# Optimization experiments

Measured on AMD Instinct MI355X. Metric: run time of the kernel, lower is better.

## Reference

```python
import jax, jax.numpy as jnp
import numpy as np

BN_EPS = 1e-5
K = 16


def pairwise_sqdist(a, b):
    # a: (B,N,C), b: (B,M,C) -> (B,N,M)
    aa = jnp.sum(a * a, axis=-1)[:, :, None]
    bb = jnp.sum(b * b, axis=-1)[:, None, :]
    return aa + bb - 2.0 * jnp.einsum('bnc,bmc->bnm', a, b)


def knn_idx(pts, k):
    # pts: (B,N,C) -> (B,N,k) indices of k nearest points (incl. self)
    d = pairwise_sqdist(pts, pts)
    _, idx = jax.lax.top_k(-d, k)
    return idx


def gather_points(pts, idx):
    # pts: (B,N,C), idx: (B,N,k) -> (B,N,k,C)
    return jax.vmap(lambda p, i: p[i])(pts, idx)


def conv_bn(x, W, b, gm, bt, relu=True):
    # 1x1 Conv1d + BatchNorm1d (training-mode batch stats) [+ ReLU]
    # x: (B,Cin,N), W: (Cout,Cin)
    y = jnp.einsum('oc,bcn->bon', W, x) + b[None, :, None]
    mu = jnp.mean(y, axis=(0, 2), keepdims=True)
    var = jnp.var(y, axis=(0, 2), keepdims=True)
    y = (y - mu) / jnp.sqrt(var + BN_EPS) * gm[None, :, None] + bt[None, :, None]
    return jax.nn.relu(y) if relu else y


def graph_layer(x, W, b, gm, bt):
    # x: (B,C,N)
    ft = jnp.swapaxes(x, 1, 2)                # (B,N,C)
    idx = knn_idx(ft, K)                      # (B,N,k)
    knn_x = gather_points(ft, idx)            # (B,N,k,C)
    m = jnp.max(knn_x, axis=2)                # (B,N,C)
    return conv_bn(jnp.swapaxes(m, 1, 2), W, b, gm, bt, relu=True)


def setup_inputs() -> dict:
    key = jax.random.key(0)
    ks = jax.random.split(key, 8)
    B, N = 8, 2048
    d = {'x': jax.random.normal(ks[0], (B, N, 3), dtype=jnp.float32)}

    def conv_params(k, cout, cin):
        W = jax.random.normal(k, (cout, cin), dtype=jnp.float32) * 0.02
        return W, jnp.zeros((cout,), jnp.float32), jnp.ones((cout,), jnp.float32), jnp.zeros((cout,), jnp.float32)

    for name, k, co, ci in [('1', ks[1], 64, 12), ('2', ks[2], 64, 64), ('3', ks[3], 64, 64),
                            ('g1', ks[4], 128, 64), ('g2', ks[5], 1024, 128), ('4', ks[6], 512, 1024)]:
        W, b, gm, bt = conv_params(k, co, ci)
        d['W' + name] = W; d['b' + name] = b; d['gm' + name] = gm; d['bt' + name] = bt
    return d


def reference(x, W1, b1, gm1, bt1, W2, b2, gm2, bt2, W3, b3, gm3, bt3,
              Wg1, bg1, gmg1, btg1, Wg2, bg2, gmg2, btg2, W4, b4, gm4, bt4):
    # x: (B,N,3)
    idx = knn_idx(x, K)                       # (B,N,k)
    knn_x = gather_points(x, idx)             # (B,N,k,3)
    knn_x = knn_x - jnp.mean(knn_x, axis=2, keepdims=True)
    cov = jnp.einsum('bnkc,bnkd->bncd', knn_x, knn_x)      # (B,N,3,3)
    B, N = x.shape[0], x.shape[1]
    cov = cov.reshape(B, N, 9).transpose(0, 2, 1)          # (B,9,N)
    h = jnp.concatenate([jnp.swapaxes(x, 1, 2), cov], axis=1)  # (B,12,N)
    h = conv_bn(h, W1, b1, gm1, bt1)
    h = conv_bn(h, W2, b2, gm2, bt2)
    h = conv_bn(h, W3, b3, gm3, bt3)
    h = graph_layer(h, Wg1, bg1, gmg1, btg1)               # (B,128,N)
    h = graph_layer(h, Wg2, bg2, gmg2, btg2)               # (B,1024,N)
    h = conv_bn(h, W4, b4, gm4, bt4, relu=False)           # (B,512,N)
    return jnp.max(h, axis=-1)                             # (B,512)
```

## Files before the change

### kernel.cpp

```cpp
#include <hip/hip_runtime.h>
#include <math.h>

#define B_ 8
#define N_ 2048
#define KNN 16

typedef __attribute__((ext_vector_type(4))) float f32x4;
typedef __attribute__((ext_vector_type(8))) short bf16x8;
typedef __attribute__((ext_vector_type(8))) _Float16 f16x8;
typedef __attribute__((address_space(3))) unsigned int lds_u32_t;
typedef __attribute__((address_space(1))) const unsigned int glb_u32_t;

__device__ inline unsigned short f2bf(float f) {
    unsigned int x = __float_as_uint(f);
    unsigned int r = (x + 0x7fffu + ((x >> 16) & 1u)) >> 16;
    return (unsigned short)r;
}

__device__ inline unsigned int fflip(float f) {
    unsigned int u = __float_as_uint(f);
    return u ^ (0x80000000u | (unsigned int)((int)u >> 31));
}

__device__ inline unsigned long long shflx64(unsigned long long v, int m) {
    int lo = __shfl_xor((int)(unsigned int)(v & 0xffffffffull), m, 64);
    int hi = __shfl_xor((int)(unsigned int)(v >> 32), m, 64);
    return ((unsigned long long)(unsigned int)hi << 32) | (unsigned int)lo;
}

__device__ inline void ce(unsigned long long& a, unsigned long long& b) {
    bool c = a < b;
    unsigned long long lo = c ? a : b;
    unsigned long long hi = c ? b : a;
    a = lo;
    b = hi;
}

#define SORT16(q)                                                         \
    _Pragma("unroll") for (int kk_ = 2; kk_ <= 16; kk_ <<= 1)             \
    _Pragma("unroll") for (int jj_ = kk_ >> 1; jj_ > 0; jj_ >>= 1)        \
    _Pragma("unroll") for (int ii_ = 0; ii_ < 16; ii_++) {                \
        int ll_ = ii_ ^ jj_;                                              \
        if (ll_ > ii_) {                                                  \
            if ((ii_ & kk_) == 0) ce(q[ii_], q[ll_]);                     \
            else ce(q[ll_], q[ii_]);                                      \
        }                                                                 \
    }

#define MERGE16(q)                                                        \
    _Pragma("unroll") for (int jj_ = 8; jj_ > 0; jj_ >>= 1)               \
    _Pragma("unroll") for (int ii_ = 0; ii_ < 16; ii_++) {                \
        int ll_ = ii_ ^ jj_;                                              \
        if (ll_ > ii_) ce(q[ii_], q[ll_]);                                \
    }

#define TOP16OF32(kA, kB, q)                                              \
    SORT16(kA);                                                           \
    SORT16(kB);                                                           \
    _Pragma("unroll") for (int ii_ = 0; ii_ < 16; ii_++) {                \
        unsigned long long b_ = kB[15 - ii_];                             \
        q[ii_] = kA[ii_] < b_ ? kA[ii_] : b_;                             \
    }                                                                     \
    MERGE16(q);

#define EXTRACT16(q, op)                                                  \
    for (int r_ = 0; r_ < KNN; r_++) {                                    \
        unsigned long long mk_ = q[0];                                    \
        _Pragma("unroll") for (int s_ = 32; s_ > 0; s_ >>= 1) {           \
            unsigned long long ok_ = shflx64(mk_, s_);                    \
            if (ok_ < mk_) mk_ = ok_;                                     \
        }                                                                 \
        if (lane == 0) (op)[r_] = (int)(mk_ & 2047u);                     \
        bool pop_ = (q[0] == mk_);                                        \
        _Pragma("unroll") for (int t_ = 0; t_ < 15; t_++)                 \
            q[t_] = pop_ ? q[t_ + 1] : q[t_];                             \
        q[15] = pop_ ? ~0ull : q[15];                                     \
    }

__global__ __launch_bounds__(256, 4) void knn3_kernel(const float* __restrict__ x,
                                                      int* __restrict__ idx,
                                                      float* __restrict__ h0) {
    __shared__ float px[N_], py[N_], pz[N_];
    int b = blockIdx.y;
    const float* xb = x + (size_t)b * N_ * 3;
    for (int e = threadIdx.x; e < N_; e += 256) {
        px[e] = xb[e * 3 + 0];
        py[e] = xb[e * 3 + 1];
        pz[e] = xb[e * 3 + 2];
    }
    __syncthreads();

    int wave = threadIdx.x >> 6, lane = threadIdx.x & 63;
    int i = blockIdx.x * 4 + wave;
    float qx = px[i], qy = py[i], qz = pz[i];

    unsigned long long kA[16], kB[16];
#pragma unroll
    for (int t = 0; t < 16; t++) {
        int j = lane + t * 64;
        float dx = px[j] - qx, dy = py[j] - qy, dz = pz[j] - qz;
        float d = dx * dx + dy * dy + dz * dz;
        kA[t] = ((unsigned long long)fflip(d) << 11) | (unsigned int)j;
    }
#pragma unroll
    for (int t = 0; t < 16; t++) {
        int j = lane + (t + 16) * 64;
        float dx = px[j] - qx, dy = py[j] - qy, dz = pz[j] - qz;
        float d = dx * dx + dy * dy + dz * dz;
        kB[t] = ((unsigned long long)fflip(d) << 11) | (unsigned int)j;
    }

    unsigned long long q[16];
    TOP16OF32(kA, kB, q);

    int* op = idx + ((size_t)b * N_ + i) * KNN;
    unsigned int jr[16];
#pragma unroll
    for (int r_ = 0; r_ < KNN; r_++) {
        unsigned long long mk_ = q[0];
#pragma unroll
        for (int s_ = 32; s_ > 0; s_ >>= 1) {
            unsigned long long ok_ = shflx64(mk_, s_);
            if (ok_ < mk_) mk_ = ok_;
        }
        jr[r_] = (unsigned int)(mk_ & 2047u);
        if (lane == 0) op[r_] = (int)jr[r_];
        bool pop_ = (q[0] == mk_);
#pragma unroll
        for (int t_ = 0; t_ < 15; t_++) q[t_] = pop_ ? q[t_ + 1] : q[t_];
        q[15] = pop_ ? ~0ull : q[15];
    }

    float nx[16], ny[16], nz[16];
    float mx = 0.f, my = 0.f, mz = 0.f;
#pragma unroll
    for (int r_ = 0; r_ < 16; r_++) {
        int j = (int)jr[r_];
        nx[r_] = px[j]; ny[r_] = py[j]; nz[r_] = pz[j];
        mx += nx[r_]; my += ny[r_]; mz += nz[r_];
    }
    mx *= (1.f / KNN); my *= (1.f / KNN); mz *= (1.f / KNN);
    float c00 = 0, c01 = 0, c02 = 0, c11 = 0, c12 = 0, c22 = 0;
#pragma unroll
    for (int r_ = 0; r_ < 16; r_++) {
        float dx = nx[r_] - mx, dy = ny[r_] - my, dz = nz[r_] - mz;
        c00 += dx * dx; c01 += dx * dy; c02 += dx * dz;
        c11 += dy * dy; c12 += dy * dz; c22 += dz * dz;
    }
    if (lane == 0) {
        float* hb = h0 + (size_t)b * 12 * N_;
        hb[0 * N_ + i] = qx;
        hb[1 * N_ + i] = qy;
        hb[2 * N_ + i] = qz;
        hb[3 * N_ + i] = c00; hb[4 * N_ + i] = c01; hb[5 * N_ + i] = c02;
        hb[6 * N_ + i] = c01; hb[7 * N_ + i] = c11; hb[8 * N_ + i] = c12;
        hb[9 * N_ + i] = c02; hb[10 * N_ + i] = c12; hb[11 * N_ + i] = c22;
    }
}

__global__ __launch_bounds__(256) void gemm_kernel(const float* __restrict__ A,
                                                   const float* __restrict__ X,
                                                   const float* __restrict__ bias,
                                                   float* __restrict__ Y,
                                                   int O, int C,
                                                   float* __restrict__ part) {
    __shared__ float Wt[16][132];
    __shared__ float Xt[16][132];
    const int N = N_;
    int b = blockIdx.z;
    int oB = blockIdx.y * 128, nB = blockIdx.x * 128;
    const float* Xb = X + (size_t)b * C * N;
    int tid = threadIdx.x;
    int tn = tid & 15, to = tid >> 4;

    float acc[8][8];
#pragma unroll
    for (int i = 0; i < 8; i++)
#pragma unroll
        for (int j = 0; j < 8; j++) acc[i][j] = 0.f;

    for (int c0 = 0; c0 < C; c0 += 16) {
#pragma unroll
        for (int r = 0; r < 8; r++) {
            int e = tid + r * 256;
            int k = e & 15, o = e >> 4;
            float v = 0.f;
            if (c0 + k < C && oB + o < O) v = A[(size_t)(oB + o) * C + c0 + k];
            Wt[k][o] = v;
        }
#pragma unroll
        for (int r = 0; r < 8; r++) {
            int e = tid + r * 256;
            int n = e & 127, k = e >> 7;
            float v = 0.f;
            if (c0 + k < C) v = Xb[(size_t)(c0 + k) * N + nB + n];
            Xt[k][n] = v;
        }
        __syncthreads();
#pragma unroll
        for (int k = 0; k < 16; k++) {
            float a[8], xv[8];
#pragma unroll
            for (int i = 0; i < 8; i++) a[i] = Wt[k][to * 8 + i];
#pragma unroll
            for (int m = 0; m < 4; m++) {
                xv[2 * m] = Xt[k][tn * 2 + 32 * m];
                xv[2 * m + 1] = Xt[k][tn * 2 + 32 * m + 1];
            }
#pragma unroll
            for (int i = 0; i < 8; i++)
#pragma unroll
                for (int j = 0; j < 8; j++) acc[i][j] = fmaf(a[i], xv[j], acc[i][j]);
        }
        __syncthreads();
    }

#pragma unroll
    for (int i = 0; i < 8; i++) {
        int o = oB + to * 8 + i;
        if (o >= O) continue;
        float bv = bias[o];
        float s = 0.f, s2 = 0.f;
#pragma unroll
        for (int m = 0; m < 4; m++) {
            int n0 = nB + tn * 2 + 32 * m;
            float v0 = acc[i][2 * m] + bv, v1 = acc[i][2 * m + 1] + bv;
            *reinterpret_cast<float2*>(&Y[((size_t)b * O + o) * N + n0]) = make_float2(v0, v1);
            s += v0 + v1;
            s2 = fmaf(v0, v0, fmaf(v1, v1, s2));
        }
#pragma unroll
        for (int msk = 1; msk <= 8; msk <<= 1) {
            s += __shfl_xor(s, msk, 64);
            s2 += __shfl_xor(s2, msk, 64);
        }
        if (tn == 0) {
            float* pp = &part[((size_t)(o * 8 + b) * 16 + blockIdx.x) * 2];
            pp[0] = s; pp[1] = s2;
        }
    }
}

__global__ __launch_bounds__(256) void splitbn_kernel(const float* __restrict__ y,
                                                      const float* __restrict__ scale,
                                                      const float* __restrict__ shift,
                                                      _Float16* __restrict__ fh,
                                                      _Float16* __restrict__ fl, int O) {
    __shared__ float tile[64][65];
    int b = blockIdx.z;
    int n0 = blockIdx.x * 64, o0 = blockIdx.y * 64;
    int t = threadIdx.x;
#pragma unroll
    for (int rr = 0; rr < 16; rr++) {
        int ol = rr * 4 + (t >> 6), nl = t & 63;
        float v = y[((size_t)b * O + o0 + ol) * N_ + n0 + nl];
        v = fmaf(v, scale[o0 + ol], shift[o0 + ol]);
        tile[ol][nl] = fmaxf(v, 0.f);
    }
    __syncthreads();
#pragma unroll
    for (int rr = 0; rr < 2; rr++) {
        int e = t + rr * 256;
        int n = e >> 3, og = (e & 7) * 8;
        f16x8 hv, lv;
#pragma unroll
        for (int j = 0; j < 8; j++) {
            float v = tile[og + j][n];
            _Float16 h = (_Float16)v;
            hv[j] = h;
            lv[j] = (_Float16)(v - (float)h);
        }
        size_t off = ((size_t)b * N_ + n0 + n) * O + o0 + og;
        *reinterpret_cast<uint4*>(&fh[off]) = *reinterpret_cast<uint4*>(&hv);
        *reinterpret_cast<uint4*>(&fl[off]) = *reinterpret_cast<uint4*>(&lv);
    }
}

__global__ __launch_bounds__(256) void normsh_kernel(const _Float16* __restrict__ fh,
                                                     const _Float16* __restrict__ fl,
                                                     float* __restrict__ nrm, int C) {
    int b = blockIdx.y;
    int i = blockIdx.x * 256 + threadIdx.x;
    const _Float16* ph = fh + ((size_t)(b << 11) + i) * C;
    const _Float16* pl = fl + ((size_t)(b << 11) + i) * C;
    float s = 0.f;
    for (int c = 0; c < C; c += 8) {
        f16x8 h = *reinterpret_cast<const f16x8*>(&ph[c]);
        f16x8 l = *reinterpret_cast<const f16x8*>(&pl[c]);
#pragma unroll
        for (int q = 0; q < 8; q++) {
            float v = (float)h[q] + (float)l[q];
            s = fmaf(v, v, s);
        }
    }
    nrm[(b << 11) + i] = s;
}

__global__ __launch_bounds__(256) void dmfma_kernel(const _Float16* __restrict__ Fh,
                                                    const _Float16* __restrict__ Fl,
                                                    const float* __restrict__ nrm,
                                                    float* __restrict__ D, int C) {
    __shared__ __align__(16) char smem[65536];
    _Float16* Ah = (_Float16*)(smem);
    _Float16* Al = (_Float16*)(smem + 16384);
    _Float16* Bh = (_Float16*)(smem + 32768);
    _Float16* Bl = (_Float16*)(smem + 49152);
    float(*Tt)[132] = (float(*)[132])smem;

    int bz = blockIdx.z;
    int t = blockIdx.x;
    int bx = (int)((sqrtf(8.f * (float)t + 1.f) - 1.f) * 0.5f);
    while ((bx + 1) * (bx + 2) / 2 <= t) bx++;
    while (bx * (bx + 1) / 2 > t) bx--;
    int by = t - bx * (bx + 1) / 2;
    int oB = by * 128, nB = bx * 128;
    const _Float16* Fhb = Fh + (size_t)bz * N_ * C;
    const _Float16* Flb = Fl + (size_t)bz * N_ * C;
    const float* nb = nrm + (size_t)bz * N_;
    float* Db = D + (size_t)bz * N_ * N_;

    int tid = threadIdx.x;
    int lane = tid & 63, w = tid >> 6;
    int wm = w & 1, wn = w >> 1;
    int lr = lane & 15, lg = lane >> 4;
    int lrow = lane >> 3;
    int lcol = ((lane & 7) ^ lrow) * 8;

    f32x4 acc[4][4];
#pragma unroll
    for (int m = 0; m < 4; m++)
#pragma unroll
        for (int n = 0; n < 4; n++) acc[m][n] = (f32x4){0.f, 0.f, 0.f, 0.f};

    for (int c0 = 0; c0 < C; c0 += 64) {
#pragma unroll
        for (int r = 0; r < 4; r++) {
            int seg = r * 4 + w;
            int row = seg * 8 + lrow;
            const _Float16* gah = &Fhb[(size_t)(oB + row) * C + c0 + lcol];
            const _Float16* gal = &Flb[(size_t)(oB + row) * C + c0 + lcol];
            const _Float16* gbh = &Fhb[(size_t)(nB + row) * C + c0 + lcol];
            const _Float16* gbl = &Flb[(size_t)(nB + row) * C + c0 + lcol];
            __builtin_amdgcn_global_load_lds((glb_u32_t*)gah, (lds_u32_t*)&Ah[seg * 512], 16, 0, 0);
            __builtin_amdgcn_global_load_lds((glb_u32_t*)gal, (lds_u32_t*)&Al[seg * 512], 16, 0, 0);
            __builtin_amdgcn_global_load_lds((glb_u32_t*)gbh, (lds_u32_t*)&Bh[seg * 512], 16, 0, 0);
            __builtin_amdgcn_global_load_lds((glb_u32_t*)gbl, (lds_u32_t*)&Bl[seg * 512], 16, 0, 0);
        }
        __syncthreads();
#pragma unroll
        for (int kk = 0; kk < 2; kk++) {
            f16x8 ah[4], al[4], bh[4], bl[4];
#pragma unroll
            for (int m = 0; m < 4; m++) {
                int row = wm * 64 + m * 16 + lr;
                int slot = (kk * 4 + lg) ^ (lr & 7);
                ah[m] = *reinterpret_cast<const f16x8*>(&Ah[row * 64 + slot * 8]);
                al[m] = *reinterpret_cast<const f16x8*>(&Al[row * 64 + slot * 8]);
            }
#pragma unroll
            for (int n = 0; n < 4; n++) {
                int row = wn * 64 + n * 16 + lr;
                int slot = (kk * 4 + lg) ^ (lr & 7);
                bh[n] = *reinterpret_cast<const f16x8*>(&Bh[row * 64 + slot * 8]);
                bl[n] = *reinterpret_cast<const f16x8*>(&Bl[row * 64 + slot * 8]);
            }
#pragma unroll
            for (int m = 0; m < 4; m++)
#pragma unroll
                for (int n = 0; n < 4; n++) {
                    acc[m][n] = __builtin_amdgcn_mfma_f32_16x16x32_f16(al[m], bh[n], acc[m][n], 0, 0, 0);
                    acc[m][n] = __builtin_amdgcn_mfma_f32_16x16x32_f16(ah[m], bl[n], acc[m][n], 0, 0, 0);
                    acc[m][n] = __builtin_amdgcn_mfma_f32_16x16x32_f16(ah[m], bh[n], acc[m][n], 0, 0, 0);
                }
        }
        __syncthreads();
    }

#pragma unroll
    for (int m = 0; m < 4; m++) {
#pragma unroll
        for (int r = 0; r < 4; r++) {
            int o = oB + wm * 64 + m * 16 + lg * 4 + r;
            float nr_ = nb[o];
#pragma unroll
            for (int n = 0; n < 4; n++) {
                int nv = nB + wn * 64 + n * 16 + lr;
                float val = nr_ + nb[nv] - 2.f * acc[m][n][r];
                unsigned int fk = fflip(val);
                Db[(size_t)o * N_ + nv] = __uint_as_float(fk);
                acc[m][n][r] = __uint_as_float(fk);
            }
        }
    }

    if (bx != by) {
        for (int p = 0; p < 4; p++) {
            __syncthreads();
            if (wm == (p >> 1)) {
#pragma unroll
                for (int mh = 0; mh < 2; mh++) {
                    int m = (p & 1) * 2 + mh;
                    int ib = m * 16 + lg * 4 - (p & 1) * 32;
#pragma unroll
                    for (int n = 0; n < 4; n++) {
                        int j = wn * 64 + n * 16 + lr;
#pragma unroll
                        for (int r = 0; r < 4; r++) Tt[ib + r][j] = acc[m][n][r];
                    }
                }
            }
            __syncthreads();
#pragma unroll
            for (int r = 0; r < 4; r++) {
                int e = tid + r * 256;
                int j = e >> 3, i4 = e & 7;
                float4 v;
                v.x = Tt[i4 * 4 + 0][j];
                v.y = Tt[i4 * 4 + 1][j];
                v.z = Tt[i4 * 4 + 2][j];
                v.w = Tt[i4 * 4 + 3][j];
                *reinterpret_cast<float4*>(&Db[(size_t)(nB + j) * N_ + oB + p * 32 + i4 * 4]) = v;
            }
        }
    }
}

template <int XLAYOUT, int FUSE, int DUALT>
__global__ __launch_bounds__(256, 4) void cgemm_kernel(const float* __restrict__ A,
                                                       const float* __restrict__ X,
                                                       const float* __restrict__ bias,
                                                       float* __restrict__ Y,
                                                       int O, int C,
                                                       const float* __restrict__ xs,
                                                       const float* __restrict__ xh,
                                                       float* __restrict__ Yt,
                                                       float* __restrict__ part) {
    __shared__ float Wt[32][68];
    __shared__ float Xt[32][68];
    int b = blockIdx.z;
    int oB = blockIdx.y * 64, nB = blockIdx.x * 64;
    const float* Xb = X + (XLAYOUT == 0 ? (size_t)b * C * N_ : (size_t)b * N_ * C);
    int tid = threadIdx.x;
    int tn = tid & 15, to = tid >> 4;

    float acc[4][4];
#pragma unroll
    for (int i = 0; i < 4; i++)
#pragma unroll
        for (int j = 0; j < 4; j++) acc[i][j] = 0.f;

    for (int c0 = 0; c0 < C; c0 += 32) {
#pragma unroll
        for (int r = 0; r < 2; r++) {
            int e = tid + r * 256;
            int row = e >> 3, c4 = e & 7;
            float4 v = *reinterpret_cast<const float4*>(&A[(size_t)(oB + row) * C + c0 + c4 * 4]);
            Wt[c4 * 4 + 0][row] = v.x;
            Wt[c4 * 4 + 1][row] = v.y;
            Wt[c4 * 4 + 2][row] = v.z;
            Wt[c4 * 4 + 3][row] = v.w;
        }
        if (XLAYOUT == 0) {
#pragma unroll
            for (int r = 0; r < 2; r++) {
                int e = tid + r * 256;
                int k = e >> 4, n4 = e & 15;
                float4 v = *reinterpret_cast<const float4*>(&Xb[(size_t)(c0 + k) * N_ + nB + n4 * 4]);
                if (FUSE) {
                    float sc = xs[c0 + k], sh = xh[c0 + k];
                    v.x = fmaxf(fmaf(v.x, sc, sh), 0.f);
                    v.y = fmaxf(fmaf(v.y, sc, sh), 0.f);
                    v.z = fmaxf(fmaf(v.z, sc, sh), 0.f);
                    v.w = fmaxf(fmaf(v.w, sc, sh), 0.f);
                }
                *reinterpret_cast<float4*>(&Xt[k][n4 * 4]) = v;
            }
        } else {
#pragma unroll
            for (int r = 0; r < 2; r++) {
                int e = tid + r * 256;
                int n = e >> 3, c4 = e & 7;
                float4 v = *reinterpret_cast<const float4*>(&Xb[(size_t)(nB + n) * C + c0 + c4 * 4]);
                Xt[c4 * 4 + 0][n] = v.x;
                Xt[c4 * 4 + 1][n] = v.y;
                Xt[c4 * 4 + 2][n] = v.z;
                Xt[c4 * 4 + 3][n] = v.w;
            }
        }
        __syncthreads();
#pragma unroll
        for (int k = 0; k < 32; k++) {
            float a[4], xv[4];
            *reinterpret_cast<float4*>(&a[0]) = *reinterpret_cast<const float4*>(&Wt[k][to * 4]);
            *reinterpret_cast<float4*>(&xv[0]) = *reinterpret_cast<const float4*>(&Xt[k][tn * 4]);
#pragma unroll
            for (int i = 0; i < 4; i++)
#pragma unroll
                for (int j = 0; j < 4; j++) acc[i][j] = fmaf(a[i], xv[j], acc[i][j]);
        }
        __syncthreads();
    }

    float fin[4][4];
#pragma unroll
    for (int i = 0; i < 4; i++) {
        float bv = bias[oB + to * 4 + i];
#pragma unroll
        for (int j = 0; j < 4; j++) fin[i][j] = acc[i][j] + bv;
    }
#pragma unroll
    for (int i = 0; i < 4; i++) {
        int o = oB + to * 4 + i;
        int n0 = nB + tn * 4;
        float4 st;
        st.x = fin[i][0]; st.y = fin[i][1]; st.z = fin[i][2]; st.w = fin[i][3];
        *reinterpret_cast<float4*>(&Y[((size_t)b * O + o) * N_ + n0]) = st;
    }
    if (DUALT) {
#pragma unroll
        for (int j = 0; j < 4; j++) {
            int n = nB + tn * 4 + j;
            float4 st;
            st.x = fin[0][j]; st.y = fin[1][j]; st.z = fin[2][j]; st.w = fin[3][j];
            *reinterpret_cast<float4*>(&Yt[((size_t)b * N_ + n) * (size_t)O + oB + to * 4]) = st;
        }
    }
#pragma unroll
    for (int i = 0; i < 4; i++) {
        float s = (fin[i][0] + fin[i][1]) + (fin[i][2] + fin[i][3]);
        float s2 = fmaf(fin[i][0], fin[i][0], fmaf(fin[i][1], fin[i][1],
                   fmaf(fin[i][2], fin[i][2], fin[i][3] * fin[i][3])));
#pragma unroll
        for (int msk = 1; msk <= 8; msk <<= 1) {
            s += __shfl_xor(s, msk, 64);
            s2 += __shfl_xor(s2, msk, 64);
        }
        if (tn == 0) {
            int o = oB + to * 4 + i;
            float* pp = &part[((size_t)(o * 8 + b) * 32 + blockIdx.x) * 2];
            pp[0] = s; pp[1] = s2;
        }
    }
}

template <int EPI>
__global__ __launch_bounds__(256) void mgemm_kernel(const unsigned short* __restrict__ A,
                                                    const unsigned short* __restrict__ X,
                                                    const float* __restrict__ bias,
                                                    float* __restrict__ Y,
                                                    int O, int C,
                                                    float* __restrict__ part) {
    __shared__ unsigned short At[128 * 64];
    __shared__ unsigned short Bt[128 * 64];
    __shared__ float sred[2][2][64][4];
    int b = blockIdx.z;
    int oB = blockIdx.y * 128, nB = blockIdx.x * 128;
    const unsigned short* Xb = X + (size_t)b * N_ * C;
    int tid = threadIdx.x;
    int lane = tid & 63, w = tid >> 6;
    int wm = w & 1, wn = w >> 1;
    int lr = lane & 15, lg = lane >> 4;
    int lrow = lane >> 3;
    int lcol = ((lane & 7) ^ lrow) * 8;

    f32x4 acc[4][4];
#pragma unroll
    for (int m = 0; m < 4; m++)
#pragma unroll
        for (int n = 0; n < 4; n++) acc[m][n] = (f32x4){0.f, 0.f, 0.f, 0.f};

    for (int c0 = 0; c0 < C; c0 += 64) {
#pragma unroll
        for (int r = 0; r < 4; r++) {
            int seg = r * 4 + w;
            int row = seg * 8 + lrow;
            const unsigned short* ga = &A[(size_t)(oB + row) * C + c0 + lcol];
            const unsigned short* gb = &Xb[(size_t)(nB + row) * C + c0 + lcol];
            __builtin_amdgcn_global_load_lds((glb_u32_t*)ga, (lds_u32_t*)&At[seg * 512], 16, 0, 0);
            __builtin_amdgcn_global_load_lds((glb_u32_t*)gb, (lds_u32_t*)&Bt[seg * 512], 16, 0, 0);
        }
        __syncthreads();
#pragma unroll
        for (int kk = 0; kk < 2; kk++) {
            bf16x8 af[4], bfv[4];
#pragma unroll
            for (int m = 0; m < 4; m++) {
                int row = wm * 64 + m * 16 + lr;
                int slot = (kk * 4 + lg) ^ (lr & 7);
                af[m] = *reinterpret_cast<const bf16x8*>(&At[row * 64 + slot * 8]);
            }
#pragma unroll
            for (int n = 0; n < 4; n++) {
                int row = wn * 64 + n * 16 + lr;
                int slot = (kk * 4 + lg) ^ (lr & 7);
                bfv[n] = *reinterpret_cast<const bf16x8*>(&Bt[row * 64 + slot * 8]);
            }
#pragma unroll
            for (int m = 0; m < 4; m++)
#pragma unroll
                for (int n = 0; n < 4; n++)
                    acc[m][n] = __builtin_amdgcn_mfma_f32_16x16x32_bf16(af[m], bfv[n], acc[m][n], 0, 0, 0);
        }
        __syncthreads();
    }

    if (EPI == 1) {
#pragma unroll
        for (int m = 0; m < 4; m++) {
#pragma unroll
            for (int r = 0; r < 4; r++) {
                float v0 = acc[m][0][r], v1 = acc[m][1][r];
                float v2 = acc[m][2][r], v3 = acc[m][3][r];
                float mx = fmaxf(fmaxf(v0, v1), fmaxf(v2, v3));
                float mn = fminf(fminf(v0, v1), fminf(v2, v3));
                float s = (v0 + v1) + (v2 + v3);
                float s2 = fmaf(v0, v0, fmaf(v1, v1, fmaf(v2, v2, v3 * v3)));
#pragma unroll
                for (int msk = 1; msk <= 8; msk <<= 1) {
                    mx = fmaxf(mx, __shfl_xor(mx, msk, 64));
                    mn = fminf(mn, __shfl_xor(mn, msk, 64));
                    s += __shfl_xor(s, msk, 64);
                    s2 += __shfl_xor(s2, msk, 64);
                }
                if (lr == 0) {
                    int ol = m * 16 + lg * 4 + r;
                    sred[wm][wn][ol][0] = mx;
                    sred[wm][wn][ol][1] = mn;
                    sred[wm][wn][ol][2] = s;
                    sred[wm][wn][ol][3] = s2;
                }
            }
        }
        __syncthreads();
        if (tid < 128) {
            int wmv = tid >> 6, ol = tid & 63;
            float mx = fmaxf(sred[wmv][0][ol][0], sred[wmv][1][ol][0]);
            float mn = fminf(sred[wmv][0][ol][1], sred[wmv][1][ol][1]);
            float s = sred[wmv][0][ol][2] + sred[wmv][1][ol][2];
            float s2 = sred[wmv][0][ol][3] + sred[wmv][1][ol][3];
            int o = oB + wmv * 64 + ol;
            float* pp = &part[((size_t)(o * 8 + b) * 16 + blockIdx.x) * 4];
            pp[0] = mx; pp[1] = mn; pp[2] = s; pp[3] = s2;
        }
    } else {
#pragma unroll
        for (int m = 0; m < 4; m++) {
            int o0 = oB + wm * 64 + m * 16 + lg * 4;
            float4 bv = *reinterpret_cast<const float4*>(&bias[o0]);
            float s[4] = {0.f, 0.f, 0.f, 0.f};
            float s2[4] = {0.f, 0.f, 0.f, 0.f};
#pragma unroll
            for (int n = 0; n < 4; n++) {
                int nv = nB + wn * 64 + n * 16 + lr;
                float4 st;
                st.x = acc[m][n][0] + bv.x;
                st.y = acc[m][n][1] + bv.y;
                st.z = acc[m][n][2] + bv.z;
                st.w = acc[m][n][3] + bv.w;
                *reinterpret_cast<float4*>(&Y[((size_t)b * N_ + nv) * (size_t)O + o0]) = st;
                s[0] += st.x; s2[0] = fmaf(st.x, st.x, s2[0]);
                s[1] += st.y; s2[1] = fmaf(st.y, st.y, s2[1]);
                s[2] += st.z; s2[2] = fmaf(st.z, st.z, s2[2]);
                s[3] += st.w; s2[3] = fmaf(st.w, st.w, s2[3]);
            }
#pragma unroll
            for (int r = 0; r < 4; r++) {
#pragma unroll
                for (int msk = 1; msk <= 8; msk <<= 1) {
                    s[r] += __shfl_xor(s[r], msk, 64);
                    s2[r] += __shfl_xor(s2[r], msk, 64);
                }
                if (lr == 0) {
                    int ol = m * 16 + lg * 4 + r;
                    sred[wm][wn][ol][0] = s[r];
                    sred[wm][wn][ol][1] = s2[r];
                }
            }
        }
        __syncthreads();
        if (tid < 128) {
            int wmv = tid >> 6, ol = tid & 63;
            float s = sred[wmv][0][ol][0] + sred[wmv][1][ol][0];
            float s2 = sred[wmv][0][ol][1] + sred[wmv][1][ol][1];
            int o = oB + wmv * 64 + ol;
            float* pp = &part[((size_t)(o * 8 + b) * 16 + blockIdx.x) * 2];
            pp[0] = s; pp[1] = s2;
        }
    }
}

__global__ __launch_bounds__(128) void bnfin_kernel(const float* __restrict__ part,
                                                    const float* __restrict__ gm,
                                                    const float* __restrict__ bt,
                                                    float* __restrict__ scale,
                                                    float* __restrict__ shift) {
    int o = blockIdx.x;
    int t = threadIdx.x;
    const float* p = &part[((size_t)(o * 8 + (t >> 4)) * 16 + (t & 15)) * 2];
    float s = p[0], s2 = p[1];
#pragma unroll
    for (int msk = 1; msk <= 32; msk <<= 1) {
        s += __shfl_xor(s, msk, 64);
        s2 += __shfl_xor(s2, msk, 64);
    }
    __shared__ float red[4];
    int wv = t >> 6, lane = t & 63;
    if (lane == 0) { red[wv] = s; red[2 + wv] = s2; }
    __syncthreads();
    if (t == 0) {
        float S = red[0] + red[1], S2 = red[2] + red[3];
        float mu = S * (1.f / (B_ * N_));
        float var = S2 * (1.f / (B_ * N_)) - mu * mu;
        float inv = 1.f / sqrtf(var + 1e-5f);
        float sc = gm[o] * inv;
        scale[o] = sc;
        shift[o] = fmaf(-mu, sc, bt[o]);
    }
}

__global__ __launch_bounds__(256) void bnfin32_kernel(const float* __restrict__ part,
                                                      const float* __restrict__ gm,
                                                      const float* __restrict__ bt,
                                                      float* __restrict__ scale,
                                                      float* __restrict__ shift) {
    int o = blockIdx.x;
    int t = threadIdx.x;
    const float* p = &part[((size_t)(o * 8 + (t >> 5)) * 32 + (t & 31)) * 2];
    float s = p[0], s2 = p[1];
#pragma unroll
    for (int msk = 1; msk <= 32; msk <<= 1) {
        s += __shfl_xor(s, msk, 64);
        s2 += __shfl_xor(s2, msk, 64);
    }
    __shared__ float red[8];
    int wv = t >> 6, lane = t & 63;
    if (lane == 0) { red[wv] = s; red[4 + wv] = s2; }
    __syncthreads();
    if (t == 0) {
        float S = (red[0] + red[1]) + (red[2] + red[3]);
        float S2 = (red[4] + red[5]) + (red[6] + red[7]);
        float mu = S * (1.f / (B_ * N_));
        float var = S2 * (1.f / (B_ * N_)) - mu * mu;
        float inv = 1.f / sqrtf(var + 1e-5f);
        float sc = gm[o] * inv;
        scale[o] = sc;
        shift[o] = fmaf(-mu, sc, bt[o]);
    }
}

__global__ __launch_bounds__(256) void applycvt_kernel(const float* __restrict__ yt,
                                                       const float* __restrict__ scale,
                                                       const float* __restrict__ shift,
                                                       unsigned short* __restrict__ outh) {
    size_t i = ((size_t)blockIdx.x * 256 + threadIdx.x) * 8;
    int o = (int)(i & 1023u);
    float4 a = *reinterpret_cast<const float4*>(&yt[i]);
    float4 c = *reinterpret_cast<const float4*>(&yt[i + 4]);
    float4 s0 = *reinterpret_cast<const float4*>(&scale[o]);
    float4 s1 = *reinterpret_cast<const float4*>(&scale[o + 4]);
    float4 h0 = *reinterpret_cast<const float4*>(&shift[o]);
    float4 h1 = *reinterpret_cast<const float4*>(&shift[o + 4]);
    unsigned short u[8];
    u[0] = f2bf(fmaxf(fmaf(a.x, s0.x, h0.x), 0.f));
    u[1] = f2bf(fmaxf(fmaf(a.y, s0.y, h0.y), 0.f));
    u[2] = f2bf(fmaxf(fmaf(a.z, s0.z, h0.z), 0.f));
    u[3] = f2bf(fmaxf(fmaf(a.w, s0.w, h0.w), 0.f));
    u[4] = f2bf(fmaxf(fmaf(c.x, s1.x, h1.x), 0.f));
    u[5] = f2bf(fmaxf(fmaf(c.y, s1.y, h1.y), 0.f));
    u[6] = f2bf(fmaxf(fmaf(c.z, s1.z, h1.z), 0.f));
    u[7] = f2bf(fmaxf(fmaf(c.w, s1.w, h1.w), 0.f));
    uint4 pk;
    pk.x = (unsigned)u[0] | ((unsigned)u[1] << 16);
    pk.y = (unsigned)u[2] | ((unsigned)u[3] << 16);
    pk.z = (unsigned)u[4] | ((unsigned)u[5] << 16);
    pk.w = (unsigned)u[6] | ((unsigned)u[7] << 16);
    *reinterpret_cast<uint4*>(&outh[i]) = pk;
}

__global__ __launch_bounds__(128) void bnmax_kernel(const float* __restrict__ part,
                                                    const float* __restrict__ gm,
                                                    const float* __restrict__ bt,
                                                    float* __restrict__ out) {
    int o = blockIdx.x;
    int t = threadIdx.x;
    int b = t >> 4, nb = t & 15;
    const float* p = &part[((size_t)(o * 8 + b) * 16 + nb) * 4];
    float mx = p[0], mn = p[1], s = p[2], s2 = p[3];

    float ss = s, ss2 = s2;
#pragma unroll
    for (int msk = 1; msk <= 32; msk <<= 1) {
        ss += __shfl_xor(ss, msk, 64);
        ss2 += __shfl_xor(ss2, msk, 64);
    }
    __shared__ float red[4];
    int wv = t >> 6, lane = t & 63;
    if (lane == 0) { red[wv] = ss; red[2 + wv] = ss2; }
    __syncthreads();
    float S = red[0] + red[1], S2 = red[2] + red[3];
    float mu = S * (1.f / (B_ * N_));
    float var = S2 * (1.f / (B_ * N_)) - mu * mu;
    float inv = 1.f / sqrtf(var + 1e-5f);
    float sc = gm[o] * inv;
    float sh = fmaf(-mu, sc, bt[o]);

#pragma unroll
    for (int msk = 1; msk <= 8; msk <<= 1) {
        mx = fmaxf(mx, __shfl_xor(mx, msk, 64));
        mn = fminf(mn, __shfl_xor(mn, msk, 64));
    }
    if (nb == 0) out[b * 512 + o] = fmaf(sc, sc >= 0.f ? mx : mn, sh);
}

__global__ __launch_bounds__(256, 4) void topk_kernel(const float* __restrict__ D,
                                                      int* __restrict__ idx) {
    int wave = threadIdx.x >> 6, lane = threadIdx.x & 63;
    int i = blockIdx.x * 4 + wave;
    const unsigned int* dp = (const unsigned int*)(D + (size_t)i * N_);

    unsigned long long kA[16], kB[16];
#pragma unroll
    for (int t = 0; t < 4; t++) {
        uint4 v = *reinterpret_cast<const uint4*>(&dp[t * 256 + lane * 4]);
        int j0 = t * 256 + lane * 4;
        kA[t * 4 + 0] = ((unsigned long long)v.x << 11) | (unsigned int)(j0 + 0);
        kA[t * 4 + 1] = ((unsigned long long)v.y << 11) | (unsigned int)(j0 + 1);
        kA[t * 4 + 2] = ((unsigned long long)v.z << 11) | (unsigned int)(j0 + 2);
        kA[t * 4 + 3] = ((unsigned long long)v.w << 11) | (unsigned int)(j0 + 3);
    }
#pragma unroll
    for (int t = 4; t < 8; t++) {
        uint4 v = *reinterpret_cast<const uint4*>(&dp[t * 256 + lane * 4]);
        int j0 = t * 256 + lane * 4;
        kB[(t - 4) * 4 + 0] = ((unsigned long long)v.x << 11) | (unsigned int)(j0 + 0);
        kB[(t - 4) * 4 + 1] = ((unsigned long long)v.y << 11) | (unsigned int)(j0 + 1);
        kB[(t - 4) * 4 + 2] = ((unsigned long long)v.z << 11) | (unsigned int)(j0 + 2);
        kB[(t - 4) * 4 + 3] = ((unsigned long long)v.w << 11) | (unsigned int)(j0 + 3);
    }

    unsigned long long q[16];
    TOP16OF32(kA, kB, q);

    int* op = idx + (size_t)i * KNN;
    EXTRACT16(q, op);
}

__global__ __launch_bounds__(256) void gathermax_kernel(const float* __restrict__ ftraw,
                                                        const int* __restrict__ idx,
                                                        const float* __restrict__ scale,
                                                        const float* __restrict__ shift,
                                                        float* __restrict__ out, int cLog) {
    int C = 1 << cLog;
    int b = blockIdx.y;
    int nb = (blockIdx.x << (8 - cLog)) + (threadIdx.x >> cLog);
    int c = threadIdx.x & (C - 1);
    float sc = scale[c], sh = shift[c];
    const int* ip = idx + (((size_t)b << 11) + nb) * KNN;
    float m = -3.4e38f;
#pragma unroll
    for (int k = 0; k < KNN; k++) {
        int j = ip[k];
        float v = ftraw[(((size_t)b << 11) + j) * C + c];
        m = fmaxf(m, fmaxf(fmaf(v, sc, sh), 0.f));
    }
    out[(((size_t)b << 11) + nb) * C + c] = m;
}

__global__ __launch_bounds__(256) void gmaxh2_kernel(const float* __restrict__ ftraw,
                                                     const int* __restrict__ idx,
                                                     const float* __restrict__ scale,
                                                     const float* __restrict__ shift,
                                                     unsigned short* __restrict__ out) {
    const int C = 128;
    int b = blockIdx.y;
    int nb = blockIdx.x * 16 + (threadIdx.x >> 4);
    int cc = (threadIdx.x & 15) * 8;
    float4 s0 = *reinterpret_cast<const float4*>(&scale[cc]);
    float4 s1 = *reinterpret_cast<const float4*>(&scale[cc + 4]);
    float4 h0 = *reinterpret_cast<const float4*>(&shift[cc]);
    float4 h1 = *reinterpret_cast<const float4*>(&shift[cc + 4]);
    const int* ip = idx + (((size_t)b << 11) + nb) * KNN;
    float m[8];
#pragma unroll
    for (int q = 0; q < 8; q++) m[q] = -3.4e38f;
#pragma unroll
    for (int k = 0; k < KNN; k++) {
        int j = ip[k];
        const float* p = &ftraw[(((size_t)b << 11) + j) * C + cc];
        float4 a = *reinterpret_cast<const float4*>(p);
        float4 c2 = *reinterpret_cast<const float4*>(p + 4);
        m[0] = fmaxf(m[0], fmaxf(fmaf(a.x, s0.x, h0.x), 0.f));
        m[1] = fmaxf(m[1], fmaxf(fmaf(a.y, s0.y, h0.y), 0.f));
        m[2] = fmaxf(m[2], fmaxf(fmaf(a.z, s0.z, h0.z), 0.f));
        m[3] = fmaxf(m[3], fmaxf(fmaf(a.w, s0.w, h0.w), 0.f));
        m[4] = fmaxf(m[4], fmaxf(fmaf(c2.x, s1.x, h1.x), 0.f));
        m[5] = fmaxf(m[5], fmaxf(fmaf(c2.y, s1.y, h1.y), 0.f));
        m[6] = fmaxf(m[6], fmaxf(fmaf(c2.z, s1.z, h1.z), 0.f));
        m[7] = fmaxf(m[7], fmaxf(fmaf(c2.w, s1.w, h1.w), 0.f));
    }
    unsigned short u[8];
#pragma unroll
    for (int q = 0; q < 8; q++) u[q] = f2bf(m[q]);
    uint4 pk;
    pk.x = (unsigned)u[0] | ((unsigned)u[1] << 16);
    pk.y = (unsigned)u[2] | ((unsigned)u[3] << 16);
    pk.z = (unsigned)u[4] | ((unsigned)u[5] << 16);
    pk.w = (unsigned)u[6] | ((unsigned)u[7] << 16);
    *reinterpret_cast<uint4*>(&out[(((size_t)b << 11) + nb) * C + cc]) = pk;
}

__global__ __launch_bounds__(256) void wcvt2_kernel(const float* __restrict__ w1,
                                                    unsigned short* __restrict__ o1, int c1,
                                                    const float* __restrict__ w2,
                                                    unsigned short* __restrict__ o2, int c2) {
    int i = blockIdx.x * 256 + threadIdx.x;
    if (i < c1) o1[i] = f2bf(w1[i]);
    else if (i < c1 + c2) o2[i - c1] = f2bf(w2[i - c1]);
}

extern "C" void kernel_launch(void* const* d_in, const int* in_sizes, int n_in,
                              void* d_out, int out_size, void* d_ws, size_t ws_size,
                              hipStream_t stream) {
    const float* x = (const float*)d_in[0];
    const float* W1 = (const float*)d_in[1];
    const float* b1 = (const float*)d_in[2];
    const float* gm1 = (const float*)d_in[3];
    const float* bt1 = (const float*)d_in[4];
    const float* W2 = (const float*)d_in[5];
    const float* b2 = (const float*)d_in[6];
    const float* gm2 = (const float*)d_in[7];
    const float* bt2 = (const float*)d_in[8];
    const float* W3 = (const float*)d_in[9];
    const float* b3 = (const float*)d_in[10];
    const float* gm3 = (const float*)d_in[11];
    const float* bt3 = (const float*)d_in[12];
    const float* Wg1 = (const float*)d_in[13];
    const float* bg1 = (const float*)d_in[14];
    const float* gmg1 = (const float*)d_in[15];
    const float* btg1 = (const float*)d_in[16];
    const float* Wg2 = (const float*)d_in[17];
    const float* bg2 = (const float*)d_in[18];
    const float* gmg2 = (const float*)d_in[19];
    const float* btg2 = (const float*)d_in[20];
    const float* W4 = (const float*)d_in[21];
    const float* b4 = (const float*)d_in[22];
    const float* gm4 = (const float*)d_in[23];
    const float* bt4 = (const float*)d_in[24];
    float* out = (float*)d_out;
    (void)b4;

    if (ws_size < 154214400ull) return;
    char* base = (char*)d_ws;
    float* scale = (float*)(base + 0);
    float* shift = (float*)(base + 4096);
    float* nrm = (float*)(base + 8192);
    float* partC1 = (float*)(base + 8192);
    int* idx = (int*)(base + 73728);
    unsigned short* Wg2h = (unsigned short*)(base + 1122304);
    unsigned short* W4h = (unsigned short*)(base + 1384448);
    _Float16* Fh1 = (_Float16*)(base + 2433024);
    _Float16* Fl1 = (_Float16*)(base + 4530176);
    _Float16* Fh2 = (_Float16*)(base + 6627328);
    _Float16* Fl2 = (_Float16*)(base + 10821632);
    float* bufC = (float*)(base + 15015936);
    float* bufD8 = (float*)(base + 19210240);
    float* bufD4 = (float*)(base + 19210240);
    float* bufLt = (float*)(base + 19210240);
    unsigned short* bufLh = (unsigned short*)(base + 86319104);
    char* E = base + 119873536;
    float* partC = (float*)(E + 0);
    float* h0 = (float*)(E + 0);
    float* bufA = (float*)(E + 786432);
    float* bufB = (float*)(E + 4980736);
    float* bufM1 = (float*)(E + 13369344);
    float* bufM2 = (float*)(E + 21757952);
    unsigned short* bufM3h = (unsigned short*)(E + 30146560);
    float* part = (float*)(E + 0);

    wcvt2_kernel<<<2560, 256, 0, stream>>>(Wg2, Wg2h, 1024 * 128, W4, W4h, 512 * 1024);

    knn3_kernel<<<dim3(512, 8), 256, 0, stream>>>(x, idx, h0);

    gemm_kernel<<<dim3(16, 1, 8), 256, 0, stream>>>(W1, h0, b1, bufA, 64, 12, partC1);
    bnfin_kernel<<<64, 128, 0, stream>>>(partC1, gm1, bt1, scale, shift);

    cgemm_kernel<0, 1, 0><<<dim3(32, 1, 8), 256, 0, stream>>>(W2, bufA, b2, bufB, 64, 64, scale, shift, nullptr, partC);
    bnfin32_kernel<<<64, 256, 0, stream>>>(partC, gm2, bt2, scale, shift);

    cgemm_kernel<0, 1, 1><<<dim3(32, 1, 8), 256, 0, stream>>>(W3, bufB, b3, bufA, 64, 64, scale, shift, bufC, partC);
    bnfin32_kernel<<<64, 256, 0, stream>>>(partC, gm3, bt3, scale, shift);

    splitbn_kernel<<<dim3(32, 1, 8), 256, 0, stream>>>(bufA, scale, shift, Fh1, Fl1, 64);
    normsh_kernel<<<dim3(8, 8), 256, 0, stream>>>(Fh1, Fl1, nrm, 64);
    dmfma_kernel<<<dim3(136, 1, 8), 256, 0, stream>>>(Fh1, Fl1, nrm, bufD8, 64);
    topk_kernel<<<4096, 256, 0, stream>>>(bufD8, idx);
    gathermax_kernel<<<dim3(512, 8), 256, 0, stream>>>(bufC, idx, scale, shift, bufB, 6);

    cgemm_kernel<1, 0, 1><<<dim3(32, 2, 8), 256, 0, stream>>>(Wg1, bufB, bg1, bufM1, 128, 64, nullptr, nullptr, bufM2, partC);
    bnfin32_kernel<<<128, 256, 0, stream>>>(partC, gmg1, btg1, scale, shift);

    splitbn_kernel<<<dim3(32, 2, 8), 256, 0, stream>>>(bufM1, scale, shift, Fh2, Fl2, 128);
    normsh_kernel<<<dim3(8, 8), 256, 0, stream>>>(Fh2, Fl2, nrm, 128);
    for (int c = 0; c < 2; c++) {
        dmfma_kernel<<<dim3(136, 1, 4), 256, 0, stream>>>(
            Fh2 + (size_t)c * 4 * N_ * 128, Fl2 + (size_t)c * 4 * N_ * 128,
            nrm + (size_t)c * 4 * N_, bufD4, 128);
        topk_kernel<<<2048, 256, 0, stream>>>(bufD4, idx + (size_t)c * 4 * N_ * KNN);
    }
    gmaxh2_kernel<<<dim3(128, 8), 256, 0, stream>>>(bufM2, idx, scale, shift, bufM3h);

    mgemm_kernel<2><<<dim3(16, 8, 8), 256, 0, stream>>>(Wg2h, bufM3h, bg2, bufLt, 1024, 128, part);
    bnfin_kernel<<<1024, 128, 0, stream>>>(part, gmg2, btg2, scale, shift);
    applycvt_kernel<<<8192, 256, 0, stream>>>(bufLt, scale, shift, bufLh);

    mgemm_kernel<1><<<dim3(16, 4, 8), 256, 0, stream>>>(W4h, bufLh, nullptr, nullptr, 512, 1024, part);
    bnmax_kernel<<<512, 128, 0, stream>>>(part, gm4, bt4, out);
}
```

Baseline: 438.7 us.

## Fuse norm into splitbn, store bf16 pre-BN gemm output, drop unused knn idx write

Three separate changes. The squared-norm computation is folded into splitbn_kernel, which now loops over all channel tiles per block, so the standalone normsh kernel and its reread of fh/fl go away. The 1024-channel gemm writes its pre-BN output as bf16 instead of fp32, roughly halving that intermediate's write and read traffic in applycvt; the BN statistics are still taken from fp32 values, but the stored values lose precision before BN is applied. The first knn kernel no longer writes neighbor indices, which nothing read afterwards.

```diff
diff --git a/kernel.cpp b/kernel.cpp
--- a/kernel.cpp
+++ b/kernel.cpp
@@ -78,7 +78,6 @@
     }
 
 __global__ __launch_bounds__(256, 4) void knn3_kernel(const float* __restrict__ x,
-                                                      int* __restrict__ idx,
                                                       float* __restrict__ h0) {
     __shared__ float px[N_], py[N_], pz[N_];
     int b = blockIdx.y;
@@ -113,7 +112,6 @@
     unsigned long long q[16];
     TOP16OF32(kA, kB, q);
 
-    int* op = idx + ((size_t)b * N_ + i) * KNN;
     unsigned int jr[16];
 #pragma unroll
     for (int r_ = 0; r_ < KNN; r_++) {
@@ -124,7 +122,6 @@
             if (ok_ < mk_) mk_ = ok_;
         }
         jr[r_] = (unsigned int)(mk_ & 2047u);
-        if (lane == 0) op[r_] = (int)jr[r_];
         bool pop_ = (q[0] == mk_);
 #pragma unroll
         for (int t_ = 0; t_ < 15; t_++) q[t_] = pop_ ? q[t_ + 1] : q[t_];
@@ -241,59 +238,68 @@
     }
 }
 
+template <int NT>
 __global__ __launch_bounds__(256) void splitbn_kernel(const float* __restrict__ y,
                                                       const float* __restrict__ scale,
                                                       const float* __restrict__ shift,
                                                       _Float16* __restrict__ fh,
-                                                      _Float16* __restrict__ fl, int O) {
+                                                      _Float16* __restrict__ fl,
+                                                      float* __restrict__ nrm) {
+    const int O = NT * 64;
     __shared__ float tile[64][65];
+    __shared__ float np[64][8];
     int b = blockIdx.z;
-    int n0 = blockIdx.x * 64, o0 = blockIdx.y * 64;
+    int n0 = blockIdx.x * 64;
     int t = threadIdx.x;
-#pragma unroll
-    for (int rr = 0; rr < 16; rr++) {
-        int ol = rr * 4 + (t >> 6), nl = t & 63;
-        float v = y[((size_t)b * O + o0 + ol) * N_ + n0 + nl];
-        v = fmaf(v, scale[o0 + ol], shift[o0 + ol]);
-        tile[ol][nl] = fmaxf(v, 0.f);
+    float ps[2] = {0.f, 0.f};
+
+#pragma unroll
+    for (int ot = 0; ot < NT; ot++) {
+        int o0 = ot * 64;
+        if (ot) __syncthreads();
+#pragma unroll
+        for (int rr = 0; rr < 16; rr++) {
+            int ol = rr * 4 + (t >> 6), nl = t & 63;
+            float v = y[((size_t)b * O + o0 + ol) * N_ + n0 + nl];
+            v = fmaf(v, scale[o0 + ol], shift[o0 + ol]);
+            tile[ol][nl] = fmaxf(v, 0.f);
+        }
+        __syncthreads();
+#pragma unroll
+        for (int rr = 0; rr < 2; rr++) {
+            int e = t + rr * 256;
+            int n = e >> 3, og = (e & 7) * 8;
+            f16x8 hv, lv;
+            float s = ps[rr];
+#pragma unroll
+            for (int j = 0; j < 8; j++) {
+                float v = tile[og + j][n];
+                _Float16 h = (_Float16)v;
+                hv[j] = h;
+                _Float16 l = (_Float16)(v - (float)h);
+                lv[j] = l;
+                float vr = (float)h + (float)l;
+                s = fmaf(vr, vr, s);
+            }
+            ps[rr] = s;
+            size_t off = ((size_t)b * N_ + n0 + n) * O + o0 + og;
+            *reinterpret_cast<uint4*>(&fh[off]) = *reinterpret_cast<uint4*>(&hv);
+            *reinterpret_cast<uint4*>(&fl[off]) = *reinterpret_cast<uint4*>(&lv);
+        }
     }
     __syncthreads();
 #pragma unroll
     for (int rr = 0; rr < 2; rr++) {
         int e = t + rr * 256;
-        int n = e >> 3, og = (e & 7) * 8;
-        f16x8 hv, lv;
-#pragma unroll
-        for (int j = 0; j < 8; j++) {
-            float v = tile[og + j][n];
-            _Float16 h = (_Float16)v;
-            hv[j] = h;
-            lv[j] = (_Float16)(v - (float)h);
-        }
-        size_t off = ((size_t)b * N_ + n0 + n) * O + o0 + og;
-        *reinterpret_cast<uint4*>(&fh[off]) = *reinterpret_cast<uint4*>(&hv);
-        *reinterpret_cast<uint4*>(&fl[off]) = *reinterpret_cast<uint4*>(&lv);
-    }
-}
-
-__global__ __launch_bounds__(256) void normsh_kernel(const _Float16* __restrict__ fh,
-                                                     const _Float16* __restrict__ fl,
-                                                     float* __restrict__ nrm, int C) {
-    int b = blockIdx.y;
-    int i = blockIdx.x * 256 + threadIdx.x;
-    const _Float16* ph = fh + ((size_t)(b << 11) + i) * C;
-    const _Float16* pl = fl + ((size_t)(b << 11) + i) * C;
-    float s = 0.f;
-    for (int c = 0; c < C; c += 8) {
-        f16x8 h = *reinterpret_cast<const f16x8*>(&ph[c]);
-        f16x8 l = *reinterpret_cast<const f16x8*>(&pl[c]);
-#pragma unroll
-        for (int q = 0; q < 8; q++) {
-            float v = (float)h[q] + (float)l[q];
-            s = fmaf(v, v, s);
-        }
-    }
-    nrm[(b << 11) + i] = s;
+        np[e >> 3][e & 7] = ps[rr];
+    }
+    __syncthreads();
+    if (t < 64) {
+        float s = 0.f;
+#pragma unroll
+        for (int g = 0; g < 8; g++) s += np[t][g];
+        nrm[(b << 11) + n0 + t] = s;
+    }
 }
 
 __global__ __launch_bounds__(256) void dmfma_kernel(const _Float16* __restrict__ Fh,
@@ -547,7 +553,7 @@
 __global__ __launch_bounds__(256) void mgemm_kernel(const unsigned short* __restrict__ A,
                                                     const unsigned short* __restrict__ X,
                                                     const float* __restrict__ bias,
-                                                    float* __restrict__ Y,
+                                                    unsigned short* __restrict__ Yh,
                                                     int O, int C,
                                                     float* __restrict__ part) {
     __shared__ unsigned short At[128 * 64];
@@ -652,16 +658,18 @@
 #pragma unroll
             for (int n = 0; n < 4; n++) {
                 int nv = nB + wn * 64 + n * 16 + lr;
-                float4 st;
-                st.x = acc[m][n][0] + bv.x;
-                st.y = acc[m][n][1] + bv.y;
-                st.z = acc[m][n][2] + bv.z;
-                st.w = acc[m][n][3] + bv.w;
-                *reinterpret_cast<float4*>(&Y[((size_t)b * N_ + nv) * (size_t)O + o0]) = st;
-                s[0] += st.x; s2[0] = fmaf(st.x, st.x, s2[0]);
-                s[1] += st.y; s2[1] = fmaf(st.y, st.y, s2[1]);
-                s[2] += st.z; s2[2] = fmaf(st.z, st.z, s2[2]);
-                s[3] += st.w; s2[3] = fmaf(st.w, st.w, s2[3]);
+                float v0 = acc[m][n][0] + bv.x;
+                float v1 = acc[m][n][1] + bv.y;
+                float v2 = acc[m][n][2] + bv.z;
+                float v3 = acc[m][n][3] + bv.w;
+                uint2 pk;
+                pk.x = (unsigned)f2bf(v0) | ((unsigned)f2bf(v1) << 16);
+                pk.y = (unsigned)f2bf(v2) | ((unsigned)f2bf(v3) << 16);
+                *reinterpret_cast<uint2*>(&Yh[((size_t)b * N_ + nv) * (size_t)O + o0]) = pk;
+                s[0] += v0; s2[0] = fmaf(v0, v0, s2[0]);
+                s[1] += v1; s2[1] = fmaf(v1, v1, s2[1]);
+                s[2] += v2; s2[2] = fmaf(v2, v2, s2[2]);
+                s[3] += v3; s2[3] = fmaf(v3, v3, s2[3]);
             }
 #pragma unroll
             for (int r = 0; r < 4; r++) {
@@ -748,27 +756,28 @@
     }
 }
 
-__global__ __launch_bounds__(256) void applycvt_kernel(const float* __restrict__ yt,
+__global__ __launch_bounds__(256) void applycvt_kernel(const unsigned short* __restrict__ yh,
                                                        const float* __restrict__ scale,
                                                        const float* __restrict__ shift,
                                                        unsigned short* __restrict__ outh) {
     size_t i = ((size_t)blockIdx.x * 256 + threadIdx.x) * 8;
     int o = (int)(i & 1023u);
-    float4 a = *reinterpret_cast<const float4*>(&yt[i]);
-    float4 c = *reinterpret_cast<const float4*>(&yt[i + 4]);
+    uint4 v = *reinterpret_cast<const uint4*>(&yh[i]);
     float4 s0 = *reinterpret_cast<const float4*>(&scale[o]);
     float4 s1 = *reinterpret_cast<const float4*>(&scale[o + 4]);
     float4 h0 = *reinterpret_cast<const float4*>(&shift[o]);
     float4 h1 = *reinterpret_cast<const float4*>(&shift[o + 4]);
+    unsigned int wv[4] = {v.x, v.y, v.z, v.w};
+    float sc[8] = {s0.x, s0.y, s0.z, s0.w, s1.x, s1.y, s1.z, s1.w};
+    float sh[8] = {h0.x, h0.y, h0.z, h0.w, h1.x, h1.y, h1.z, h1.w};
     unsigned short u[8];
-    u[0] = f2bf(fmaxf(fmaf(a.x, s0.x, h0.x), 0.f));
-    u[1] = f2bf(fmaxf(fmaf(a.y, s0.y, h0.y), 0.f));
-    u[2] = f2bf(fmaxf(fmaf(a.z, s0.z, h0.z), 0.f));
-    u[3] = f2bf(fmaxf(fmaf(a.w, s0.w, h0.w), 0.f));
-    u[4] = f2bf(fmaxf(fmaf(c.x, s1.x, h1.x), 0.f));
-    u[5] = f2bf(fmaxf(fmaf(c.y, s1.y, h1.y), 0.f));
-    u[6] = f2bf(fmaxf(fmaf(c.z, s1.z, h1.z), 0.f));
-    u[7] = f2bf(fmaxf(fmaf(c.w, s1.w, h1.w), 0.f));
+#pragma unroll
+    for (int q = 0; q < 4; q++) {
+        float lo = __uint_as_float(wv[q] << 16);
+        float hi = __uint_as_float(wv[q] & 0xffff0000u);
+        u[2 * q] = f2bf(fmaxf(fmaf(lo, sc[2 * q], sh[2 * q]), 0.f));
+        u[2 * q + 1] = f2bf(fmaxf(fmaf(hi, sc[2 * q + 1], sh[2 * q + 1]), 0.f));
+    }
     uint4 pk;
     pk.x = (unsigned)u[0] | ((unsigned)u[1] << 16);
     pk.y = (unsigned)u[2] | ((unsigned)u[3] << 16);
@@ -965,7 +974,7 @@
     float* bufC = (float*)(base + 15015936);
     float* bufD8 = (float*)(base + 19210240);
     float* bufD4 = (float*)(base + 19210240);
-    float* bufLt = (float*)(base + 19210240);
+    unsigned short* bufLrh = (unsigned short*)(base + 19210240);
     unsigned short* bufLh = (unsigned short*)(base + 86319104);
     char* E = base + 119873536;
     float* partC = (float*)(E + 0);
@@ -979,7 +988,7 @@
 
     wcvt2_kernel<<<2560, 256, 0, stream>>>(Wg2, Wg2h, 1024 * 128, W4, W4h, 512 * 1024);
 
-    knn3_kernel<<<dim3(512, 8), 256, 0, stream>>>(x, idx, h0);
+    knn3_kernel<<<dim3(512, 8), 256, 0, stream>>>(x, h0);
 
     gemm_kernel<<<dim3(16, 1, 8), 256, 0, stream>>>(W1, h0, b1, bufA, 64, 12, partC1);
     bnfin_kernel<<<64, 128, 0, stream>>>(partC1, gm1, bt1, scale, shift);
@@ -990,8 +999,7 @@
     cgemm_kernel<0, 1, 1><<<dim3(32, 1, 8), 256, 0, stream>>>(W3, bufB, b3, bufA, 64, 64, scale, shift, bufC, partC);
     bnfin32_kernel<<<64, 256, 0, stream>>>(partC, gm3, bt3, scale, shift);
 
-    splitbn_kernel<<<dim3(32, 1, 8), 256, 0, stream>>>(bufA, scale, shift, Fh1, Fl1, 64);
-    normsh_kernel<<<dim3(8, 8), 256, 0, stream>>>(Fh1, Fl1, nrm, 64);
+    splitbn_kernel<1><<<dim3(32, 1, 8), 256, 0, stream>>>(bufA, scale, shift, Fh1, Fl1, nrm);
     dmfma_kernel<<<dim3(136, 1, 8), 256, 0, stream>>>(Fh1, Fl1, nrm, bufD8, 64);
     topk_kernel<<<4096, 256, 0, stream>>>(bufD8, idx);
     gathermax_kernel<<<dim3(512, 8), 256, 0, stream>>>(bufC, idx, scale, shift, bufB, 6);
@@ -999,8 +1007,7 @@
     cgemm_kernel<1, 0, 1><<<dim3(32, 2, 8), 256, 0, stream>>>(Wg1, bufB, bg1, bufM1, 128, 64, nullptr, nullptr, bufM2, partC);
     bnfin32_kernel<<<128, 256, 0, stream>>>(partC, gmg1, btg1, scale, shift);
 
-    splitbn_kernel<<<dim3(32, 2, 8), 256, 0, stream>>>(bufM1, scale, shift, Fh2, Fl2, 128);
-    normsh_kernel<<<dim3(8, 8), 256, 0, stream>>>(Fh2, Fl2, nrm, 128);
+    splitbn_kernel<2><<<dim3(32, 1, 8), 256, 0, stream>>>(bufM1, scale, shift, Fh2, Fl2, nrm);
     for (int c = 0; c < 2; c++) {
         dmfma_kernel<<<dim3(136, 1, 4), 256, 0, stream>>>(
             Fh2 + (size_t)c * 4 * N_ * 128, Fl2 + (size_t)c * 4 * N_ * 128,
@@ -1009,9 +1016,9 @@
     }
     gmaxh2_kernel<<<dim3(128, 8), 256, 0, stream>>>(bufM2, idx, scale, shift, bufM3h);
 
-    mgemm_kernel<2><<<dim3(16, 8, 8), 256, 0, stream>>>(Wg2h, bufM3h, bg2, bufLt, 1024, 128, part);
+    mgemm_kernel<2><<<dim3(16, 8, 8), 256, 0, stream>>>(Wg2h, bufM3h, bg2, bufLrh, 1024, 128, part);
     bnfin_kernel<<<1024, 128, 0, stream>>>(part, gmg2, btg2, scale, shift);
-    applycvt_kernel<<<8192, 256, 0, stream>>>(bufLt, scale, shift, bufLh);
+    applycvt_kernel<<<8192, 256, 0, stream>>>(bufLrh, scale, shift, bufLh);
 
     mgemm_kernel<1><<<dim3(16, 4, 8), 256, 0, stream>>>(W4h, bufLh, nullptr, nullptr, 512, 1024, part);
     bnmax_kernel<<<512, 128, 0, stream>>>(part, gm4, bt4, out);
```

New measurement: 426.5 us. -2.8%, faster.
